# Kernel optimization log

Measured on AMD Instinct MI355X. Metric: run time of the kernel, lower is better.

## Reference

```python
import jax, jax.numpy as jnp
import numpy as np

H = 128
B, N = 8, 200
EPS = 1e-5


def _linear(v, W, b):
    return v @ W.T + b


def _masked_bn(v, m, gamma, beta):
    # v: (..., H); m: (...,) float 0/1 mask. BatchNorm1d over masked rows only
    # (track_running_stats=False -> batch statistics, biased variance).
    mf = m[..., None]
    axes = tuple(range(v.ndim - 1))
    cnt = jnp.maximum(jnp.sum(m), 1.0)
    mean = jnp.sum(v * mf, axis=axes) / cnt            # (H,)
    var = jnp.sum(mf * (v - mean) ** 2, axis=axes) / cnt
    vn = (v - mean) * jax.lax.rsqrt(var + EPS) * gamma + beta
    return jnp.where(mf > 0, vn, v)


def setup_inputs() -> dict:
    key = jax.random.key(0)
    ks = jax.random.split(key, 16)
    s = 1.0 / np.sqrt(H)
    p = lambda k, shp: jax.random.uniform(k, shp, jnp.float32, -s, s)
    return {
        "x": jax.random.normal(ks[0], (B, N, H), jnp.float32),
        "e": jax.random.normal(ks[1], (B, N, N, H), jnp.float32),
        "mask": jax.random.randint(ks[2], (B, N), 0, 2, jnp.int32),
        "Ue_W": p(ks[3], (H, H)), "Ue_b": p(ks[4], (H,)),
        "Ve_W": p(ks[5], (H, H)), "Ve_b": p(ks[6], (H,)),
        "Un_W": p(ks[7], (H, H)), "Un_b": p(ks[8], (H,)),
        "Vn_W": p(ks[9], (H, H)), "Vn_b": p(ks[10], (H,)),
        "bn_n_g": jnp.ones((H,), jnp.float32), "bn_n_b": jnp.zeros((H,), jnp.float32),
        "bn_e_g": jnp.ones((H,), jnp.float32), "bn_e_b": jnp.zeros((H,), jnp.float32),
    }


def reference(x, e, mask, Ue_W, Ue_b, Ve_W, Ve_b, Un_W, Un_b, Vn_W, Vn_b,
              bn_n_g, bn_n_b, bn_e_g, bn_e_b):
    m = mask.astype(x.dtype)                      # (B,N)
    m1 = m[..., None]                             # (B,N,1)
    sq_mask = m[:, :, None] * m[:, None, :]       # (B,N,N)

    # EdgeFeatures: e_ij = U*e_ij + V*x_i + V*x_j (with node-masked Vx)
    Vx = m1 * _linear(x, Ve_W, Ve_b)              # (B,N,H)
    e_tmp = _linear(e, Ue_W, Ue_b) + Vx[:, :, None, :] + Vx[:, None, :, :]

    gate = jax.nn.sigmoid(e_tmp)                  # (B,N,N,H)
    gate_m = gate * sq_mask[..., None]            # mask rows and cols

    # NodeFeatures, sum aggregation: x_i = U*x_i + sum_j gate_ij * (V*x_j)
    Ux = m1 * _linear(x, Un_W, Un_b)
    Vxn = m1 * _linear(x, Vn_W, Vn_b)
    agg = jnp.einsum("bijh,bjh->bih", gate_m, Vxn)
    x_tmp = Ux + agg

    e_bn = _masked_bn(e_tmp, sq_mask, bn_e_g, bn_e_b)
    x_bn = _masked_bn(x_tmp, m, bn_n_g, bn_n_b)

    x_new = x + jax.nn.relu(x_bn)
    e_new = e + jax.nn.relu(e_bn)
    return x_new, e_new
```

## Files before the change

kernel.cpp:

```cpp
#include <hip/hip_runtime.h>
#include <hip/hip_bf16.h>

namespace {

typedef __attribute__((ext_vector_type(8))) short short8;
typedef __attribute__((ext_vector_type(4))) float f32x4;

constexpr int H = 128;
constexpr int N = 200;
constexpr int BN = 1600;
constexpr int X_SIZE = BN * H;
constexpr int NH = N * H;

constexpr int WS_VX    = 0;
constexpr int WS_UX    = WS_VX + X_SIZE;
constexpr int WS_VXN   = WS_UX + X_SIZE;
constexpr int WS_XTMP  = WS_VXN + X_SIZE;
constexpr int WS_ESUMS = WS_XTMP + X_SIZE;
constexpr int WS_ESSQS = WS_ESUMS + 32 * H;
constexpr int WS_NSUMS = WS_ESSQS + 32 * H;
constexpr int WS_NSSQS = WS_NSUMS + 32 * H;
constexpr int WS_STAT_END = WS_NSSQS + 32 * H;
constexpr int WS_ESC   = WS_STAT_END;
constexpr int WS_ESH   = WS_ESC + H;
constexpr int WS_NSC   = WS_ESH + H;
constexpr int WS_NSH   = WS_NSC + H;

__device__ __forceinline__ unsigned short f2bf(float f) {
  __hip_bfloat16 h = __float2bfloat16(f);
  return __builtin_bit_cast(unsigned short, h);
}

__device__ __forceinline__ short8 pack8(f32x4 a, f32x4 b) {
  short8 r;
  r[0] = (short)f2bf(a[0]); r[1] = (short)f2bf(a[1]);
  r[2] = (short)f2bf(a[2]); r[3] = (short)f2bf(a[3]);
  r[4] = (short)f2bf(b[0]); r[5] = (short)f2bf(b[1]);
  r[6] = (short)f2bf(b[2]); r[7] = (short)f2bf(b[3]);
  return r;
}

__global__ __launch_bounds__(128) void k_prep(
    const float* __restrict__ x, const int* __restrict__ mask,
    const float* __restrict__ VeW, const float* __restrict__ Veb,
    const float* __restrict__ UnW, const float* __restrict__ Unb,
    const float* __restrict__ VnW, const float* __restrict__ Vnb,
    float* __restrict__ ws) {
  const int bi = blockIdx.x, h = threadIdx.x;
  __shared__ float xr[H];
  xr[h] = x[bi * H + h];
  __syncthreads();
  const float mi = (float)mask[bi];
  float a0 = 0.f, a1 = 0.f, a2 = 0.f;
  #pragma unroll 4
  for (int k = 0; k < H; k += 4) {
    const float x0 = xr[k], x1 = xr[k + 1], x2 = xr[k + 2], x3 = xr[k + 3];
    float4 w;
    w = *(const float4*)&VeW[h * H + k];
    a0 += w.x * x0 + w.y * x1 + w.z * x2 + w.w * x3;
    w = *(const float4*)&UnW[h * H + k];
    a1 += w.x * x0 + w.y * x1 + w.z * x2 + w.w * x3;
    w = *(const float4*)&VnW[h * H + k];
    a2 += w.x * x0 + w.y * x1 + w.z * x2 + w.w * x3;
  }
  ws[WS_VX  + bi * H + h] = mi * (a0 + Veb[h]);
  ws[WS_UX  + bi * H + h] = mi * (a1 + Unb[h]);
  ws[WS_VXN + bi * H + h] = mi * (a2 + Vnb[h]);
}

__global__ __launch_bounds__(256, 3) void k_edge0(
    const float* __restrict__ e, const int* __restrict__ mask,
    const float* __restrict__ UeW, const float* __restrict__ Ueb,
    float* __restrict__ ws) {
  const int bi = blockIdx.x;
  const int b = bi / N;
  const int tid = threadIdx.x;
  const int w = tid >> 6, lane = tid & 63;
  const int l15 = lane & 15, lg = lane >> 4;
  const int hbase = w * 32;

  __shared__ float lds[2][3 * 2048];
  __shared__ float mrow[N];
  __shared__ float sS[H], sS2[H], sA[H];

  const float mi = (float)mask[bi];
  const float* __restrict__ eg  = e + (size_t)bi * NH;
  const float* __restrict__ vxg = ws + WS_VX  + (size_t)b * NH;
  const float* __restrict__ vng = ws + WS_VXN + (size_t)b * NH;

  auto stage = [&](int buf, int jt) {
    const int j0 = jt * 16;
    #pragma unroll
    for (int ii = 0; ii < 2; ++ii) {
      const int instr = 2 * w + ii;
      const int row = 2 * instr + (lane >> 5);
      const int gr = min(j0 + row, N - 1);
      const int sc16 = (lane & 31) ^ (row & 7);
      const size_t so = (size_t)gr * H + sc16 * 4;
      float* dst = &lds[buf][instr * 256];
      __builtin_amdgcn_global_load_lds(
          (const __attribute__((address_space(1))) void*)(eg + so),
          (__attribute__((address_space(3))) void*)dst, 16, 0, 0);
      __builtin_amdgcn_global_load_lds(
          (const __attribute__((address_space(1))) void*)(vxg + so),
          (__attribute__((address_space(3))) void*)(dst + 2048), 16, 0, 0);
      __builtin_amdgcn_global_load_lds(
          (const __attribute__((address_space(1))) void*)(vng + so),
          (__attribute__((address_space(3))) void*)(dst + 4096), 16, 0, 0);
    }
  };

  stage(0, 0);
  if (tid < N) mrow[tid] = (float)mask[b * N + tid];

  short8 Wf[2][4];
  #pragma unroll
  for (int ht = 0; ht < 2; ++ht) {
    const float* wr = &UeW[(size_t)(hbase + ht * 16 + l15) * H + lg * 8];
    #pragma unroll
    for (int s = 0; s < 4; ++s) {
      const f32x4 u0 = *(const f32x4*)(wr + s * 32);
      const f32x4 u1 = *(const f32x4*)(wr + s * 32 + 4);
      Wf[ht][s] = pack8(u0, u1);
    }
  }
  f32x4 base4[2];
  #pragma unroll
  for (int ht = 0; ht < 2; ++ht) {
    const int h0 = hbase + ht * 16 + 4 * lg;
    const f32x4 ub = *(const f32x4*)&Ueb[h0];
    const f32x4 vx = *(const f32x4*)&ws[WS_VX + (size_t)bi * H + h0];
    base4[ht] = ub + vx;
  }

  float bnS[2][4] = {{0,0,0,0},{0,0,0,0}};
  float bnS2[2][4] = {{0,0,0,0},{0,0,0,0}};
  float ag[2][4] = {{0,0,0,0},{0,0,0,0}};

  __syncthreads();

  for (int jt = 0; jt < 13; ++jt) {
    const int cur = jt & 1;
    if (jt + 1 < 13) stage(cur ^ 1, jt + 1);

    const float* tp = &lds[cur][0];
    short8 Ef[4];
    #pragma unroll
    for (int s = 0; s < 4; ++s) {
      const int c0 = (lg * 2 + s * 8) ^ (l15 & 7);
      const int c1 = (lg * 2 + s * 8 + 1) ^ (l15 & 7);
      const f32x4 u0 = *(const f32x4*)&tp[l15 * 128 + c0 * 4];
      const f32x4 u1 = *(const f32x4*)&tp[l15 * 128 + c1 * 4];
      Ef[s] = pack8(u0, u1);
    }

    f32x4 acc[2] = {f32x4(0.f), f32x4(0.f)};
    #pragma unroll
    for (int s = 0; s < 4; ++s) {
      #pragma unroll
      for (int ht = 0; ht < 2; ++ht)
        acc[ht] = __builtin_amdgcn_mfma_f32_16x16x32_bf16(Wf[ht][s], Ef[s], acc[ht], 0, 0, 0);
    }

    const int j = jt * 16 + l15;
    const bool valid = (j < N);
    const float msk = valid ? mi * mrow[valid ? j : 0] : 0.f;
    #pragma unroll
    for (int ht = 0; ht < 2; ++ht) {
      const int h0 = hbase + ht * 16 + 4 * lg;
      const int ch = (h0 >> 2) ^ (l15 & 7);
      const f32x4 vx4 = *(const f32x4*)&tp[2048 + l15 * 128 + ch * 4];
      const f32x4 vn4 = *(const f32x4*)&tp[4096 + l15 * 128 + ch * 4];
      #pragma unroll
      for (int r = 0; r < 4; ++r) {
        const float v = acc[ht][r] + base4[ht][r] + vx4[r];
        bnS[ht][r]  += msk * v;
        bnS2[ht][r] += msk * v * v;
        const float sg = __builtin_amdgcn_rcpf(1.f + __expf(-v));
        ag[ht][r] += msk * sg * vn4[r];
      }
    }
    __syncthreads();
  }

  #pragma unroll
  for (int ht = 0; ht < 2; ++ht) {
    #pragma unroll
    for (int r = 0; r < 4; ++r) {
      #pragma unroll
      for (int mm = 1; mm <= 8; mm <<= 1) {
        bnS[ht][r]  += __shfl_xor(bnS[ht][r], mm);
        bnS2[ht][r] += __shfl_xor(bnS2[ht][r], mm);
        ag[ht][r]   += __shfl_xor(ag[ht][r], mm);
      }
    }
  }
  if (l15 == 0) {
    #pragma unroll
    for (int ht = 0; ht < 2; ++ht) {
      #pragma unroll
      for (int r = 0; r < 4; ++r) {
        const int h = hbase + ht * 16 + 4 * lg + r;
        sS[h] = bnS[ht][r]; sS2[h] = bnS2[ht][r]; sA[h] = ag[ht][r];
      }
    }
  }
  __syncthreads();
  if (tid < H) {
    const int slot = (bi & 31) * H + tid;
    atomicAdd(&ws[WS_ESUMS + slot], sS[tid]);
    atomicAdd(&ws[WS_ESSQS + slot], sS2[tid]);
    const float v = ws[WS_UX + (size_t)bi * H + tid] + sA[tid];
    ws[WS_XTMP + (size_t)bi * H + tid] = v;
    atomicAdd(&ws[WS_NSUMS + slot], mi * v);
    atomicAdd(&ws[WS_NSSQS + slot], mi * v * v);
  }
}

__global__ void k_stats(const int* __restrict__ mask,
                        const float* __restrict__ beg, const float* __restrict__ beb,
                        const float* __restrict__ bng, const float* __restrict__ bnb,
                        float* __restrict__ ws) {
  __shared__ float sb[8];
  const int t = threadIdx.x;
  const int b = t >> 5, li = t & 31;
  float s = 0.f;
  for (int i = li; i < N; i += 32) s += (float)mask[b * N + i];
  #pragma unroll
  for (int o = 16; o >= 1; o >>= 1) s += __shfl_down(s, o, 32);
  if (li == 0) sb[b] = s;
  __syncthreads();
  if (t < H) {
    float cn = 0.f, ce = 0.f;
    #pragma unroll
    for (int bb = 0; bb < 8; ++bb) { cn += sb[bb]; ce += sb[bb] * sb[bb]; }
    ce = fmaxf(ce, 1.f); cn = fmaxf(cn, 1.f);
    float es = 0.f, es2 = 0.f, ns = 0.f, ns2 = 0.f;
    #pragma unroll 4
    for (int k = 0; k < 32; ++k) {
      es  += ws[WS_ESUMS + k * H + t];
      es2 += ws[WS_ESSQS + k * H + t];
      ns  += ws[WS_NSUMS + k * H + t];
      ns2 += ws[WS_NSSQS + k * H + t];
    }
    const float me = es / ce;
    const float ve = fmaxf(es2 / ce - me * me, 0.f);
    const float se = rsqrtf(ve + 1e-5f) * beg[t];
    ws[WS_ESC + t] = se;
    ws[WS_ESH + t] = beb[t] - me * se;
    const float mn = ns / cn;
    const float vn = fmaxf(ns2 / cn - mn * mn, 0.f);
    const float sn = rsqrtf(vn + 1e-5f) * bng[t];
    ws[WS_NSC + t] = sn;
    ws[WS_NSH + t] = bnb[t] - mn * sn;
  }
}

__global__ void k_x2(const float* __restrict__ x, const int* __restrict__ mask,
                     const float* __restrict__ ws, float* __restrict__ out) {
  const int idx = blockIdx.x * 256 + threadIdx.x;
  if (idx >= X_SIZE) return;
  const int h = idx & 127, bi = idx >> 7;
  const float v = ws[WS_XTMP + idx];
  const float r = (mask[bi] != 0) ? (v * ws[WS_NSC + h] + ws[WS_NSH + h]) : v;
  out[idx] = x[idx] + fmaxf(r, 0.f);
}

__global__ __launch_bounds__(256, 3) void k_edge1(
    const float* __restrict__ e, const int* __restrict__ mask,
    const float* __restrict__ UeW, const float* __restrict__ Ueb,
    const float* __restrict__ ws, float* __restrict__ out) {
  const int bi = blockIdx.x;
  const int b = bi / N;
  const int tid = threadIdx.x;
  const int w = tid >> 6, lane = tid & 63;
  const int l15 = lane & 15, lg = lane >> 4;
  const int hbase = w * 32;

  __shared__ float lds[2][2 * 2048];
  __shared__ float mrow[N];

  const float mi = (float)mask[bi];
  const float* __restrict__ eg  = e + (size_t)bi * NH;
  const float* __restrict__ vxg = ws + WS_VX + (size_t)b * NH;

  auto stage = [&](int buf, int jt) {
    const int j0 = jt * 16;
    #pragma unroll
    for (int ii = 0; ii < 2; ++ii) {
      const int instr = 2 * w + ii;
      const int row = 2 * instr + (lane >> 5);
      const int gr = min(j0 + row, N - 1);
      const int sc16 = (lane & 31) ^ (row & 7);
      const size_t so = (size_t)gr * H + sc16 * 4;
      float* dst = &lds[buf][instr * 256];
      __builtin_amdgcn_global_load_lds(
          (const __attribute__((address_space(1))) void*)(eg + so),
          (__attribute__((address_space(3))) void*)dst, 16, 0, 0);
      __builtin_amdgcn_global_load_lds(
          (const __attribute__((address_space(1))) void*)(vxg + so),
          (__attribute__((address_space(3))) void*)(dst + 2048), 16, 0, 0);
    }
  };

  stage(0, 0);
  if (tid < N) mrow[tid] = (float)mask[b * N + tid];

  short8 Wf[2][4];
  #pragma unroll
  for (int ht = 0; ht < 2; ++ht) {
    const float* wr = &UeW[(size_t)(hbase + ht * 16 + l15) * H + lg * 8];
    #pragma unroll
    for (int s = 0; s < 4; ++s) {
      const f32x4 u0 = *(const f32x4*)(wr + s * 32);
      const f32x4 u1 = *(const f32x4*)(wr + s * 32 + 4);
      Wf[ht][s] = pack8(u0, u1);
    }
  }
  f32x4 base4[2], sc4[2], sh4[2];
  #pragma unroll
  for (int ht = 0; ht < 2; ++ht) {
    const int h0 = hbase + ht * 16 + 4 * lg;
    const f32x4 ub = *(const f32x4*)&Ueb[h0];
    const f32x4 vx = *(const f32x4*)&ws[WS_VX + (size_t)bi * H + h0];
    base4[ht] = ub + vx;
    sc4[ht] = *(const f32x4*)&ws[WS_ESC + h0];
    sh4[ht] = *(const f32x4*)&ws[WS_ESH + h0];
  }

  __syncthreads();

  for (int jt = 0; jt < 13; ++jt) {
    const int cur = jt & 1;
    if (jt + 1 < 13) stage(cur ^ 1, jt + 1);

    const float* tp = &lds[cur][0];
    short8 Ef[4];
    #pragma unroll
    for (int s = 0; s < 4; ++s) {
      const int c0 = (lg * 2 + s * 8) ^ (l15 & 7);
      const int c1 = (lg * 2 + s * 8 + 1) ^ (l15 & 7);
      const f32x4 u0 = *(const f32x4*)&tp[l15 * 128 + c0 * 4];
      const f32x4 u1 = *(const f32x4*)&tp[l15 * 128 + c1 * 4];
      Ef[s] = pack8(u0, u1);
    }

    f32x4 acc[2] = {f32x4(0.f), f32x4(0.f)};
    #pragma unroll
    for (int s = 0; s < 4; ++s) {
      #pragma unroll
      for (int ht = 0; ht < 2; ++ht)
        acc[ht] = __builtin_amdgcn_mfma_f32_16x16x32_bf16(Wf[ht][s], Ef[s], acc[ht], 0, 0, 0);
    }

    const int j = jt * 16 + l15;
    if (j < N) {
      const float msk = mi * mrow[j];
      float* __restrict__ og = out + (size_t)X_SIZE + (size_t)bi * NH + (size_t)j * H;
      #pragma unroll
      for (int ht = 0; ht < 2; ++ht) {
        const int h0 = hbase + ht * 16 + 4 * lg;
        const int ch = (h0 >> 2) ^ (l15 & 7);
        const f32x4 vx4 = *(const f32x4*)&tp[2048 + l15 * 128 + ch * 4];
        const f32x4 e4  = *(const f32x4*)&tp[l15 * 128 + ch * 4];
        f32x4 o;
        #pragma unroll
        for (int r = 0; r < 4; ++r) {
          const float v = acc[ht][r] + base4[ht][r] + vx4[r];
          const float rr = (msk > 0.f) ? (v * sc4[ht][r] + sh4[ht][r]) : v;
          o[r] = e4[r] + fmaxf(rr, 0.f);
        }
        *(f32x4*)&og[h0] = o;
      }
    }
    __syncthreads();
  }
}

}

extern "C" void kernel_launch(void* const* d_in, const int* in_sizes, int n_in,
                              void* d_out, int out_size, void* d_ws, size_t ws_size,
                              hipStream_t stream) {
  const float* x    = (const float*)d_in[0];
  const float* e    = (const float*)d_in[1];
  const int*   mask = (const int*)d_in[2];
  const float* UeW  = (const float*)d_in[3];
  const float* Ueb  = (const float*)d_in[4];
  const float* VeW  = (const float*)d_in[5];
  const float* Veb  = (const float*)d_in[6];
  const float* UnW  = (const float*)d_in[7];
  const float* Unb  = (const float*)d_in[8];
  const float* VnW  = (const float*)d_in[9];
  const float* Vnb  = (const float*)d_in[10];
  const float* bng  = (const float*)d_in[11];
  const float* bnb  = (const float*)d_in[12];
  const float* beg  = (const float*)d_in[13];
  const float* beb  = (const float*)d_in[14];
  float* ws  = (float*)d_ws;
  float* out = (float*)d_out;

  hipMemsetAsync(ws + WS_ESUMS, 0, (WS_STAT_END - WS_ESUMS) * sizeof(float), stream);
  k_prep<<<BN, 128, 0, stream>>>(x, mask, VeW, Veb, UnW, Unb, VnW, Vnb, ws);
  k_edge0<<<BN, 256, 0, stream>>>(e, mask, UeW, Ueb, ws);
  k_stats<<<1, 256, 0, stream>>>(mask, beg, beb, bng, bnb, ws);
  k_x2<<<800, 256, 0, stream>>>(x, mask, ws, out);
  k_edge1<<<BN, 256, 0, stream>>>(e, mask, UeW, Ueb, ws, out);
}
```

Before: 194.7 us.

## Prefetch two tiles ahead with explicit vmcnt waits in edge kernels

Both edge-pass kernels now issue async global-to-LDS loads for tiles 0 and 1 up front. Each iteration waits with a partial vmcnt for the current tile instead of a full __syncthreads, reads all needed LDS data into registers, then barriers and refills the freed buffer with tile jt+2 before the MFMA and epilogue. This deepens the load pipeline so global latency is hidden behind compute. It relies on hand-counted vmcnt values matching the compiler's emitted load order, including any global stores in the second kernel, which is fragile and could race if the counts are wrong.

New measurement: 189.8 us. 2.5% less time.

```diff
diff --git a/kernel.cpp b/kernel.cpp
--- a/kernel.cpp
+++ b/kernel.cpp
@@ -110,7 +110,6 @@
     }
   };
 
-  stage(0, 0);
   if (tid < N) mrow[tid] = (float)mask[b * N + tid];
 
   short8 Wf[2][4];
@@ -133,17 +132,22 @@
     base4[ht] = ub + vx;
   }
 
+  asm volatile("s_waitcnt vmcnt(0) lgkmcnt(0)" ::: "memory");
+  __builtin_amdgcn_s_barrier();
+
+  stage(0, 0);
+  stage(1, 1);
+
   float bnS[2][4] = {{0,0,0,0},{0,0,0,0}};
   float bnS2[2][4] = {{0,0,0,0},{0,0,0,0}};
   float ag[2][4] = {{0,0,0,0},{0,0,0,0}};
 
-  __syncthreads();
-
   for (int jt = 0; jt < 13; ++jt) {
-    const int cur = jt & 1;
-    if (jt + 1 < 13) stage(cur ^ 1, jt + 1);
-
-    const float* tp = &lds[cur][0];
+    if (jt < 12) asm volatile("s_waitcnt vmcnt(6)" ::: "memory");
+    else         asm volatile("s_waitcnt vmcnt(0)" ::: "memory");
+    __builtin_amdgcn_s_barrier();
+
+    const float* tp = &lds[jt & 1][0];
     short8 Ef[4];
     #pragma unroll
     for (int s = 0; s < 4; ++s) {
@@ -153,34 +157,42 @@
       const f32x4 u1 = *(const f32x4*)&tp[l15 * 128 + c1 * 4];
       Ef[s] = pack8(u0, u1);
     }
-
-    f32x4 acc[2] = {f32x4(0.f), f32x4(0.f)};
-    #pragma unroll
-    for (int s = 0; s < 4; ++s) {
-      #pragma unroll
-      for (int ht = 0; ht < 2; ++ht)
-        acc[ht] = __builtin_amdgcn_mfma_f32_16x16x32_bf16(Wf[ht][s], Ef[s], acc[ht], 0, 0, 0);
-    }
-
-    const int j = jt * 16 + l15;
-    const bool valid = (j < N);
-    const float msk = valid ? mi * mrow[valid ? j : 0] : 0.f;
+    f32x4 vx4[2], vn4[2];
     #pragma unroll
     for (int ht = 0; ht < 2; ++ht) {
       const int h0 = hbase + ht * 16 + 4 * lg;
       const int ch = (h0 >> 2) ^ (l15 & 7);
-      const f32x4 vx4 = *(const f32x4*)&tp[2048 + l15 * 128 + ch * 4];
-      const f32x4 vn4 = *(const f32x4*)&tp[4096 + l15 * 128 + ch * 4];
+      vx4[ht] = *(const f32x4*)&tp[2048 + l15 * 128 + ch * 4];
+      vn4[ht] = *(const f32x4*)&tp[4096 + l15 * 128 + ch * 4];
+    }
+
+    asm volatile("s_waitcnt lgkmcnt(0)" ::: "memory");
+    __builtin_amdgcn_sched_barrier(0);
+    __builtin_amdgcn_s_barrier();
+
+    if (jt + 2 < 13) stage(jt & 1, jt + 2);
+
+    f32x4 acc[2] = {f32x4(0.f), f32x4(0.f)};
+    #pragma unroll
+    for (int s = 0; s < 4; ++s) {
+      #pragma unroll
+      for (int ht = 0; ht < 2; ++ht)
+        acc[ht] = __builtin_amdgcn_mfma_f32_16x16x32_bf16(Wf[ht][s], Ef[s], acc[ht], 0, 0, 0);
+    }
+
+    const int j = jt * 16 + l15;
+    const float msk = (j < N) ? mi * mrow[j < N ? j : 0] : 0.f;
+    #pragma unroll
+    for (int ht = 0; ht < 2; ++ht) {
       #pragma unroll
       for (int r = 0; r < 4; ++r) {
-        const float v = acc[ht][r] + base4[ht][r] + vx4[r];
+        const float v = acc[ht][r] + base4[ht][r] + vx4[ht][r];
         bnS[ht][r]  += msk * v;
         bnS2[ht][r] += msk * v * v;
         const float sg = __builtin_amdgcn_rcpf(1.f + __expf(-v));
-        ag[ht][r] += msk * sg * vn4[r];
+        ag[ht][r] += msk * sg * vn4[ht][r];
       }
     }
-    __syncthreads();
   }
 
   #pragma unroll
@@ -303,7 +315,6 @@
     }
   };
 
-  stage(0, 0);
   if (tid < N) mrow[tid] = (float)mask[b * N + tid];
 
   short8 Wf[2][4];
@@ -328,13 +339,20 @@
     sh4[ht] = *(const f32x4*)&ws[WS_ESH + h0];
   }
 
-  __syncthreads();
+  asm volatile("s_waitcnt vmcnt(0) lgkmcnt(0)" ::: "memory");
+  __builtin_amdgcn_s_barrier();
+
+  stage(0, 0);
+  stage(1, 1);
 
   for (int jt = 0; jt < 13; ++jt) {
-    const int cur = jt & 1;
-    if (jt + 1 < 13) stage(cur ^ 1, jt + 1);
-
-    const float* tp = &lds[cur][0];
+    if (jt == 0)      asm volatile("s_waitcnt vmcnt(4)" ::: "memory");
+    else if (jt == 1) asm volatile("s_waitcnt vmcnt(6)" ::: "memory");
+    else if (jt < 12) asm volatile("s_waitcnt vmcnt(8)" ::: "memory");
+    else              asm volatile("s_waitcnt vmcnt(4)" ::: "memory");
+    __builtin_amdgcn_s_barrier();
+
+    const float* tp = &lds[jt & 1][0];
     short8 Ef[4];
     #pragma unroll
     for (int s = 0; s < 4; ++s) {
@@ -344,6 +362,20 @@
       const f32x4 u1 = *(const f32x4*)&tp[l15 * 128 + c1 * 4];
       Ef[s] = pack8(u0, u1);
     }
+    f32x4 vx4[2], e4[2];
+    #pragma unroll
+    for (int ht = 0; ht < 2; ++ht) {
+      const int h0 = hbase + ht * 16 + 4 * lg;
+      const int ch = (h0 >> 2) ^ (l15 & 7);
+      vx4[ht] = *(const f32x4*)&tp[2048 + l15 * 128 + ch * 4];
+      e4[ht]  = *(const f32x4*)&tp[l15 * 128 + ch * 4];
+    }
+
+    asm volatile("s_waitcnt lgkmcnt(0)" ::: "memory");
+    __builtin_amdgcn_sched_barrier(0);
+    __builtin_amdgcn_s_barrier();
+
+    if (jt + 2 < 13) stage(jt & 1, jt + 2);
 
     f32x4 acc[2] = {f32x4(0.f), f32x4(0.f)};
     #pragma unroll
@@ -360,20 +392,16 @@
       #pragma unroll
       for (int ht = 0; ht < 2; ++ht) {
         const int h0 = hbase + ht * 16 + 4 * lg;
-        const int ch = (h0 >> 2) ^ (l15 & 7);
-        const f32x4 vx4 = *(const f32x4*)&tp[2048 + l15 * 128 + ch * 4];
-        const f32x4 e4  = *(const f32x4*)&tp[l15 * 128 + ch * 4];
         f32x4 o;
         #pragma unroll
         for (int r = 0; r < 4; ++r) {
-          const float v = acc[ht][r] + base4[ht][r] + vx4[r];
+          const float v = acc[ht][r] + base4[ht][r] + vx4[ht][r];
           const float rr = (msk > 0.f) ? (v * sc4[ht][r] + sh4[ht][r]) : v;
-          o[r] = e4[r] + fmaxf(rr, 0.f);
+          o[r] = e4[ht][r] + fmaxf(rr, 0.f);
         }
         *(f32x4*)&og[h0] = o;
       }
     }
-    __syncthreads();
   }
 }
 
```
